# Optimization experiments

Measured on AMD Instinct MI355X. Metric: run time of the kernel, lower is better.

The kernel has to match this reference:

```python
import jax, jax.numpy as jnp
import numpy as np

WINDOW_SIZE = 11
SIGMA = 1.5
WEIGHTS = np.array([0.0448, 0.2856, 0.3001, 0.2363, 0.1333], dtype=np.float32)
LEVELS = 5


def _gaussian(ws, sigma):
    x = np.arange(ws, dtype=np.float32)
    g = np.exp(-((x - ws // 2) ** 2) / (2.0 * sigma ** 2))
    return g / g.sum()


def _window3d(ws, channel):
    g = _gaussian(ws, SIGMA)
    w3 = np.einsum('i,j,k->ijk', g, g, g).astype(np.float32)  # [ws,ws,ws]
    # OIDHW, depthwise: O=channel, I=1
    return jnp.asarray(np.broadcast_to(w3[None, None], (channel, 1, ws, ws, ws)))


def _conv3d(x, w, channel):
    return jax.lax.conv_general_dilated(
        x, w, window_strides=(1, 1, 1), padding='VALID',
        dimension_numbers=('NCDHW', 'OIDHW', 'NCDHW'),
        feature_group_count=channel)


def _avg_pool3d(x):
    s = jax.lax.reduce_window(x, 0.0, jax.lax.add,
                              (1, 1, 2, 2, 2), (1, 1, 2, 2, 2), 'VALID')
    return s / 8.0


def _ssim(img1, img2, window_size):
    _, channel, d, h, w = img1.shape
    # val_range=None branch: L derived from img1 statistics
    max_val = jnp.where(jnp.max(img1) > 128, 255.0, 1.0)
    min_val = jnp.where(jnp.min(img1) < -0.5, -1.0, 0.0)
    L = max_val - min_val
    real_size = min(window_size, d, h, w)
    win = _window3d(real_size, channel)

    mu1 = _conv3d(img1, win, channel)
    mu2 = _conv3d(img2, win, channel)
    mu1_sq = mu1 * mu1
    mu2_sq = mu2 * mu2
    mu1_mu2 = mu1 * mu2
    sigma1_sq = _conv3d(img1 * img1, win, channel) - mu1_sq
    sigma2_sq = _conv3d(img2 * img2, win, channel) - mu2_sq
    sigma12 = _conv3d(img1 * img2, win, channel) - mu1_mu2

    C1 = (0.01 * L) ** 2
    C2 = (0.03 * L) ** 2
    v1 = 2.0 * sigma12 + C2
    v2 = sigma1_sq + sigma2_sq + C2
    cs = jnp.mean(v1 / v2)
    ssim_map = (2.0 * mu1_mu2 + C1) * v1 / ((mu1_sq + mu2_sq + C1) * v2)
    return jnp.mean(ssim_map), cs


def setup_inputs() -> dict:
    key = jax.random.key(0)
    k1, k2 = jax.random.split(key)
    shape = (2, 1, 192, 192, 192)
    img1 = jax.random.normal(k1, shape, dtype=jnp.float32)
    img2 = jax.random.normal(k2, shape, dtype=jnp.float32)
    return {"img1": img1, "img2": img2}


def reference(img1, img2):
    weights = jnp.asarray(WEIGHTS)
    ssims, mcs = [], []
    for _ in range(LEVELS):
        sim, cs = _ssim(img1, img2, WINDOW_SIZE)
        ssims.append(sim)
        mcs.append(cs)
        img1 = _avg_pool3d(img1)
        img2 = _avg_pool3d(img2)
    ssims = jnp.stack(ssims)
    mcs = jnp.stack(mcs)
    pow1 = mcs ** weights
    pow2 = ssims ** weights
    return jnp.prod(pow1[:-1]) * pow2[-1]
```

## Files before the change

kernel.cpp:

```cpp
#include <hip/hip_runtime.h>
#include <math.h>


typedef float f2 __attribute__((ext_vector_type(2)));
#define PKFMA(a, b, c) __builtin_elementwise_fma((a), (b), (c))

__device__ __forceinline__ f2 mkf2(float x, float y) { f2 r; r.x = x; r.y = y; return r; }

__device__ __forceinline__ unsigned enc_f(float f) {
    unsigned u = __float_as_uint(f);
    return (u & 0x80000000u) ? ~u : (u | 0x80000000u);
}
__device__ __forceinline__ float dec_f(unsigned e) {
    unsigned u = (e & 0x80000000u) ? (e ^ 0x80000000u) : ~e;
    return __uint_as_float(u);
}

__global__ void init_kernel(float* wsf) {
    unsigned* wsu = (unsigned*)wsf;
    int t = threadIdx.x;
    if (t < 10)       wsf[t] = 0.0f;
    else if (t < 15)  wsu[t] = 0xFFFFFFFFu;
    else if (t < 20)  wsu[t] = 0u;
    else if (t == 20) wsu[t] = 0u;
}

struct PyrParams {
    const float* src[2];
    float* dst[2][4];
};

__launch_bounds__(256, 4)
__global__ void pyramid_kernel(PyrParams P, float* wsf) {
    __shared__ float L1[16 * 256];
    __shared__ float L2[512];
    __shared__ float L3[64];
    __shared__ float smn[4], smx[4];
    unsigned* wsu = (unsigned*)wsf;

    const int tid = threadIdx.x;
    int blk = blockIdx.x;
    int r = blk % 216; blk /= 216;
    int batch = blk & 1;
    int im = blk >> 1;
    const int rx = r % 6, ry = (r / 6) % 6, rz = r / 36;

    const long N0 = 192L * 192 * 192;
    const float* src = P.src[im] + (long)batch * N0;
    float* d1 = P.dst[im][0] + (long)batch * 96 * 96 * 96;
    float* d2 = P.dst[im][1] + (long)batch * 48 * 48 * 48;
    float* d3 = P.dst[im][2] + (long)batch * 24 * 24 * 24;
    float* d4 = P.dst[im][3] + (long)batch * 12 * 12 * 12;

    float mnv[5], mxv[5];
#pragma unroll
    for (int l = 0; l < 5; l++) { mnv[l] = INFINITY; mxv[l] = -INFINITY; }

    {
        const int tx2 = tid & 7;
        const int ty  = (tid >> 3) & 15;
        const int zh  = tid >> 7;
        const long D = 192, D2 = 192L * 192;
        const int gx = 2 * (rx * 16) + 4 * tx2;
        const int gy = 2 * (ry * 16 + ty);
#pragma unroll 2
        for (int it = 0; it < 8; it++) {
            const int zo = 2 * it + zh;
            const int gz = 2 * (rz * 16 + zo);
            long base = (long)gz * D2 + (long)gy * D + gx;
            float4 a00 = *(const float4*)(src + base);
            float4 a01 = *(const float4*)(src + base + D);
            float4 a10 = *(const float4*)(src + base + D2);
            float4 a11 = *(const float4*)(src + base + D2 + D);
            float lo = fminf(fminf(fminf(fminf(a00.x, a00.y), fminf(a00.z, a00.w)),
                                   fminf(fminf(a01.x, a01.y), fminf(a01.z, a01.w))),
                             fminf(fminf(fminf(a10.x, a10.y), fminf(a10.z, a10.w)),
                                   fminf(fminf(a11.x, a11.y), fminf(a11.z, a11.w))));
            float hi = fmaxf(fmaxf(fmaxf(fmaxf(a00.x, a00.y), fmaxf(a00.z, a00.w)),
                                   fmaxf(fmaxf(a01.x, a01.y), fmaxf(a01.z, a01.w))),
                             fmaxf(fmaxf(fmaxf(a10.x, a10.y), fmaxf(a10.z, a10.w)),
                                   fmaxf(fmaxf(a11.x, a11.y), fmaxf(a11.z, a11.w))));
            mnv[0] = fminf(mnv[0], lo); mxv[0] = fmaxf(mxv[0], hi);
            float s0 = (a00.x + a00.y + a01.x + a01.y +
                        a10.x + a10.y + a11.x + a11.y) * 0.125f;
            float s1 = (a00.z + a00.w + a01.z + a01.w +
                        a10.z + a10.w + a11.z + a11.w) * 0.125f;
            mnv[1] = fminf(mnv[1], fminf(s0, s1));
            mxv[1] = fmaxf(mxv[1], fmaxf(s0, s1));
            *(float2*)&d1[(long)(rz * 16 + zo) * 96 * 96 +
                          (ry * 16 + ty) * 96 + (rx * 16 + 2 * tx2)] =
                make_float2(s0, s1);
            *(float2*)&L1[zo * 256 + ty * 16 + 2 * tx2] = make_float2(s0, s1);
        }
    }
    __syncthreads();

#pragma unroll
    for (int k = 0; k < 2; k++) {
        int o = tid + (k << 8);
        int x = o & 7, y = (o >> 3) & 7, z = o >> 6;
        float s = (L1[(2 * z) * 256 + (2 * y) * 16 + 2 * x] +
                   L1[(2 * z) * 256 + (2 * y) * 16 + 2 * x + 1] +
                   L1[(2 * z) * 256 + (2 * y + 1) * 16 + 2 * x] +
                   L1[(2 * z) * 256 + (2 * y + 1) * 16 + 2 * x + 1] +
                   L1[(2 * z + 1) * 256 + (2 * y) * 16 + 2 * x] +
                   L1[(2 * z + 1) * 256 + (2 * y) * 16 + 2 * x + 1] +
                   L1[(2 * z + 1) * 256 + (2 * y + 1) * 16 + 2 * x] +
                   L1[(2 * z + 1) * 256 + (2 * y + 1) * 16 + 2 * x + 1]) * 0.125f;
        mnv[2] = fminf(mnv[2], s); mxv[2] = fmaxf(mxv[2], s);
        d2[(long)(rz * 8 + z) * 48 * 48 + (ry * 8 + y) * 48 + (rx * 8 + x)] = s;
        L2[o] = s;
    }
    __syncthreads();

    if (tid < 64) {
        int x = tid & 3, y = (tid >> 2) & 3, z = tid >> 4;
        float s = (L2[(2 * z) * 64 + (2 * y) * 8 + 2 * x] +
                   L2[(2 * z) * 64 + (2 * y) * 8 + 2 * x + 1] +
                   L2[(2 * z) * 64 + (2 * y + 1) * 8 + 2 * x] +
                   L2[(2 * z) * 64 + (2 * y + 1) * 8 + 2 * x + 1] +
                   L2[(2 * z + 1) * 64 + (2 * y) * 8 + 2 * x] +
                   L2[(2 * z + 1) * 64 + (2 * y) * 8 + 2 * x + 1] +
                   L2[(2 * z + 1) * 64 + (2 * y + 1) * 8 + 2 * x] +
                   L2[(2 * z + 1) * 64 + (2 * y + 1) * 8 + 2 * x + 1]) * 0.125f;
        mnv[3] = fminf(mnv[3], s); mxv[3] = fmaxf(mxv[3], s);
        d3[(long)(rz * 4 + z) * 24 * 24 + (ry * 4 + y) * 24 + (rx * 4 + x)] = s;
        L3[tid] = s;
    }
    __syncthreads();

    if (tid < 8) {
        int x = tid & 1, y = (tid >> 1) & 1, z = tid >> 2;
        float s = (L3[(2 * z) * 16 + (2 * y) * 4 + 2 * x] +
                   L3[(2 * z) * 16 + (2 * y) * 4 + 2 * x + 1] +
                   L3[(2 * z) * 16 + (2 * y + 1) * 4 + 2 * x] +
                   L3[(2 * z) * 16 + (2 * y + 1) * 4 + 2 * x + 1] +
                   L3[(2 * z + 1) * 16 + (2 * y) * 4 + 2 * x] +
                   L3[(2 * z + 1) * 16 + (2 * y) * 4 + 2 * x + 1] +
                   L3[(2 * z + 1) * 16 + (2 * y + 1) * 4 + 2 * x] +
                   L3[(2 * z + 1) * 16 + (2 * y + 1) * 4 + 2 * x + 1]) * 0.125f;
        mnv[4] = fminf(mnv[4], s); mxv[4] = fmaxf(mxv[4], s);
        d4[(long)(rz * 2 + z) * 12 * 12 + (ry * 2 + y) * 12 + (rx * 2 + x)] = s;
    }

    const int lane = tid & 63, w = tid >> 6;
#pragma unroll
    for (int l = 0; l < 5; l++) {
        float mn = mnv[l], mx = mxv[l];
        for (int o = 32; o; o >>= 1) {
            mn = fminf(mn, __shfl_down(mn, o));
            mx = fmaxf(mx, __shfl_down(mx, o));
        }
        __syncthreads();
        if (lane == 0) { smn[w] = mn; smx[w] = mx; }
        __syncthreads();
        if (tid == 0 && im == 0) {
            for (int i = 1; i < 4; i++) { mn = fminf(mn, smn[i]); mx = fmaxf(mx, smx[i]); }
            atomicMin(&wsu[10 + l], enc_f(mn));
            atomicMax(&wsu[15 + l], enc_f(mx));
        }
    }
}

#define TSX 16
#define TSY 32
#define EXR 42
#define EXC 26
#define SPS 26
#define NPIX (EXR * EXC)
#define TPS 17

struct AllParams {
    const float* A[5];
    const float* B[5];
    float* out;
    double cnt[5];
    int D[5], O[5], zc[5], nTx[5], nTy[5];
    int blk0[6];
    float g[11];
};

__launch_bounds__(256)
__global__ void ssim_all_kernel(AllParams P, float* wsf) {
    __shared__ __align__(16) float2 S[2][EXR * SPS];
    __shared__ __align__(16) float4 TX4[2][EXR * TPS];

    const int tid = threadIdx.x;
    const int col = tid & 15;
    const int yg  = tid >> 4;

    int level = 0;
    {
        int b = blockIdx.x;
#pragma unroll
        for (int l = 1; l < 5; l++)
            if (b >= P.blk0[l]) level = l;
    }
    int rel = blockIdx.x - P.blk0[level];
    const int D   = P.D[level];
    const int O   = P.O[level];
    const int ZC  = P.zc[level];
    const int nTx = P.nTx[level];
    const int nTy = P.nTy[level];

    const int tx = rel % nTx;  rel /= nTx;
    const int ty = rel % nTy;  rel /= nTy;
    const int batch = rel & 1;
    const int chunk = rel >> 1;

    const int oz0 = chunk * ZC;
    const int oz1 = min(oz0 + ZC, O);
    const int nplanes = oz1 - oz0 + 10;
    const int ox0 = tx * TSX;
    const int oy0 = ty * TSY;
    const int D2  = D * D;
    const float* A = P.A[level] + (long)batch * D * D2;
    const float* B = P.B[level] + (long)batch * D * D2;

    const unsigned* wsu = (const unsigned*)wsf;
    float mxv = dec_f(wsu[15 + level]);
    float mnv = dec_f(wsu[10 + level]);
    float maxval = (mxv > 128.f) ? 255.f : 1.f;
    float minval = (mnv < -0.5f) ? -1.f : 0.f;
    float Lr = maxval - minval;
    float C1 = 0.01f * Lr; C1 *= C1;
    float C2 = 0.03f * Lr; C2 *= C2;

    int  poff[5], sidx[5];
    bool pval[5];
#pragma unroll
    for (int k = 0; k < 5; k++) {
        int idx = tid + (k << 8);
        pval[k] = (idx < NPIX);
        int row = idx / EXC;
        int c   = idx - row * EXC;
        sidx[k] = row * SPS + c;
        int gy = min(oy0 + row, D - 1);
        int gx = min(ox0 + c,   D - 1);
        poff[k] = gy * D + gx;
    }

    f2 Acc2[4][11] = {};
    float ssim_acc = 0.f, cs_acc = 0.f;

    const bool vx  = (ox0 + col < O);
    const bool vy0 = vx && (oy0 + 2 * yg < O);
    const bool vy1 = vx && (oy0 + 2 * yg + 1 < O);

    float2 Pld[5];
    {
        long zoff = (long)oz0 * D2;
#pragma unroll
        for (int k = 0; k < 5; k++)
            if (pval[k]) Pld[k] = make_float2(A[zoff + poff[k]], B[zoff + poff[k]]);
    }

    for (int it = 0; it < nplanes + 2; ++it) {
        if (it < nplanes) {
            float2* Sc = S[it & 1];
#pragma unroll
            for (int k = 0; k < 5; k++)
                if (pval[k]) Sc[sidx[k]] = Pld[k];
            if (it + 1 < nplanes) {
                long zoff = (long)(oz0 + it + 1) * D2;
#pragma unroll
                for (int k = 0; k < 5; k++)
                    if (pval[k]) Pld[k] = make_float2(A[zoff + poff[k]], B[zoff + poff[k]]);
            }
        }

        if (it >= 1 && it <= nplanes && tid < EXR * 4) {
            const float2* Sc = S[(it - 1) & 1];
            float4* Tc = TX4[(it - 1) & 1];
            const int row = tid >> 2;
            const int cg  = tid & 3;
            const float4* srow = (const float4*)(Sc + row * SPS);
            f2 mm[4] = {}, qq[4] = {};
#pragma unroll
            for (int i = 0; i < 7; i++) {
                float4 qv = srow[2 * cg + i];
#pragma unroll
                for (int h = 0; h < 2; h++) {
                    const int jj = 2 * i + h;
                    float a = h ? qv.z : qv.x;
                    float b = h ? qv.w : qv.y;
                    f2 ab  = mkf2(a, b);
                    float e  = a * b;
                    float s2 = fmaf(a, a, b * b);
                    f2 se2 = mkf2(s2, e);
#pragma unroll
                    for (int cc = 0; cc < 4; cc++) {
                        const int j = jj - cc;
                        if (j >= 0 && j <= 10) {
                            f2 w = mkf2(P.g[j], P.g[j]);
                            mm[cc] = PKFMA(w, ab,  mm[cc]);
                            qq[cc] = PKFMA(w, se2, qq[cc]);
                        }
                    }
                }
            }
#pragma unroll
            for (int cc = 0; cc < 4; cc++)
                Tc[row * TPS + 4 * cg + cc] =
                    make_float4(mm[cc].x, mm[cc].y, qq[cc].x, qq[cc].y);
        }

        if (it >= 2) {
            const float4* Tc = TX4[it & 1];
            f2 acc[4] = {};
#pragma unroll
            for (int j = 0; j < 12; j++) {
                float4 q = Tc[(2 * yg + j) * TPS + col];
                float we = (j < 11) ? P.g[j]     : 0.f;
                float wo = (j > 0)  ? P.g[j - 1] : 0.f;
                f2 w = mkf2(we, wo);
                acc[0] = PKFMA(w, mkf2(q.x, q.x), acc[0]);
                acc[1] = PKFMA(w, mkf2(q.y, q.y), acc[1]);
                acc[2] = PKFMA(w, mkf2(q.z, q.z), acc[2]);
                acc[3] = PKFMA(w, mkf2(q.w, q.w), acc[3]);
            }

#pragma unroll
            for (int f = 0; f < 4; f++) {
                f2 s = acc[f];
#pragma unroll
                for (int k = 0; k < 10; k++) {
                    f2 w = mkf2(P.g[10 - k], P.g[10 - k]);
                    Acc2[f][k] = PKFMA(w, s, Acc2[f][k + 1]);
                }
                Acc2[f][10] = mkf2(P.g[0], P.g[0]) * s;
            }

            if (it >= 12) {
#pragma unroll
                for (int r = 0; r < 2; r++) {
                    bool valid = r ? vy1 : vy0;
                    if (!valid) continue;
                    float m1v = r ? Acc2[0][0].y : Acc2[0][0].x;
                    float m2v = r ? Acc2[1][0].y : Acc2[1][0].x;
                    float sqv = r ? Acc2[2][0].y : Acc2[2][0].x;
                    float sbv = r ? Acc2[3][0].y : Acc2[3][0].x;
                    float mu11 = m1v * m1v, mu22 = m2v * m2v, mu12 = m1v * m2v;
                    float sg12 = sbv - mu12;
                    float sgs  = sqv - mu11 - mu22;
                    float v1 = 2.f * sg12 + C2;
                    float v2 = sgs + C2;
                    cs_acc   += v1 / v2;
                    ssim_acc += ((2.f * mu12 + C1) * v1) / ((mu11 + mu22 + C1) * v2);
                }
            }
        }

        __syncthreads();
    }

    float2* RED = (float2*)&S[0][0];
    RED[tid] = make_float2(ssim_acc, cs_acc);
    __syncthreads();
    for (int s = 128; s > 0; s >>= 1) {
        if (tid < s) {
            RED[tid].x += RED[tid + s].x;
            RED[tid].y += RED[tid + s].y;
        }
        __syncthreads();
    }
    if (tid == 0) {
        atomicAdd(&wsf[level],     RED[0].x);
        atomicAdd(&wsf[5 + level], RED[0].y);
        __threadfence();
        unsigned prev = atomicAdd((unsigned*)wsf + 20, 1u);
        if (prev == (unsigned)(P.blk0[5] - 1)) {
            double w[5];
            w[0] = (double)0.0448f; w[1] = (double)0.2856f; w[2] = (double)0.3001f;
            w[3] = (double)0.2363f; w[4] = (double)0.1333f;
            double prod = 1.0;
            for (int l = 0; l < 4; l++) {
                float cs = atomicAdd(&wsf[5 + l], 0.0f);
                prod *= pow((double)cs / P.cnt[l], w[l]);
            }
            float sm = atomicAdd(&wsf[4], 0.0f);
            prod *= pow((double)sm / P.cnt[4], w[4]);
            P.out[0] = (float)prod;
        }
    }
}

extern "C" void kernel_launch(void* const* d_in, const int* in_sizes, int n_in,
                              void* d_out, int out_size, void* d_ws, size_t ws_size,
                              hipStream_t stream) {
    (void)in_sizes; (void)n_in; (void)out_size; (void)ws_size;
    const float* img1 = (const float*)d_in[0];
    const float* img2 = (const float*)d_in[1];
    float* wsf = (float*)d_ws;
    float* out = (float*)d_out;

    const int Ds[5]  = {192, 96, 48, 24, 12};
    const int ZCs[5] = {46, 26, 14, 14, 2};

    float* bufA[5] = {nullptr};
    float* bufB[5] = {nullptr};
    size_t o = 32;
    for (int l = 1; l < 5; l++) {
        long n = 2L * Ds[l] * Ds[l] * Ds[l];
        bufA[l] = wsf + o; o += (size_t)n;
        bufB[l] = wsf + o; o += (size_t)n;
    }

    init_kernel<<<1, 64, 0, stream>>>(wsf);

    PyrParams PP;
    PP.src[0] = img1; PP.src[1] = img2;
    for (int l = 1; l < 5; l++) { PP.dst[0][l - 1] = bufA[l]; PP.dst[1][l - 1] = bufB[l]; }
    pyramid_kernel<<<216 * 2 * 2, 256, 0, stream>>>(PP, wsf);

    AllParams P;
    P.A[0] = img1; P.B[0] = img2;
    for (int l = 1; l < 5; l++) { P.A[l] = bufA[l]; P.B[l] = bufB[l]; }
    P.out = out;
    int acc = 0;
    for (int l = 0; l < 5; l++) {
        int D = Ds[l], O = D - 10, ZC = ZCs[l];
        int nTx = (O + TSX - 1) / TSX;
        int nTy = (O + TSY - 1) / TSY;
        int ZCn = (O + ZC - 1) / ZC;
        P.D[l] = D; P.O[l] = O; P.zc[l] = ZC; P.nTx[l] = nTx; P.nTy[l] = nTy;
        P.blk0[l] = acc;
        acc += nTx * nTy * 2 * ZCn;
        double Od = (double)O;
        P.cnt[l] = 2.0 * Od * Od * Od;
    }
    P.blk0[5] = acc;

    {
        float s = 0.f;
        for (int i = 0; i < 11; i++) {
            float d = (float)(i - 5);
            P.g[i] = expf(-d * d / 4.5f);
            s += P.g[i];
        }
        for (int i = 0; i < 11; i++) P.g[i] /= s;
    }

    ssim_all_kernel<<<acc, 256, 0, stream>>>(P, wsf);
}
```

Measured before the change: 303.4 us.

## Fuse pyramid into SSIM kernel with counter-based dependency and separate minmax pass

The pyramid downsampling is merged into the SSIM kernel as its first block range. Level-0 SSIM blocks can then run while pyramid blocks are still working, and level>0 blocks spin on a global completion counter. The level-0 min/max is moved into a separate grid-stride minmax kernel so level-0 SSIM no longer waits for the pyramid. This removes a kernel boundary and overlaps pyramid work with the level-0 convolution. The cost is an extra full read of img1, shared-memory union sizing, and a spin-wait that relies on pyramid blocks being scheduled before the waiting blocks.

```diff
diff --git a/kernel.cpp b/kernel.cpp
--- a/kernel.cpp
+++ b/kernel.cpp
@@ -21,144 +21,32 @@
     int t = threadIdx.x;
     if (t < 10)       wsf[t] = 0.0f;
     else if (t < 15)  wsu[t] = 0xFFFFFFFFu;
-    else if (t < 20)  wsu[t] = 0u;
-    else if (t == 20) wsu[t] = 0u;
-}
-
-struct PyrParams {
-    const float* src[2];
-    float* dst[2][4];
-};
-
-__launch_bounds__(256, 4)
-__global__ void pyramid_kernel(PyrParams P, float* wsf) {
-    __shared__ float L1[16 * 256];
-    __shared__ float L2[512];
-    __shared__ float L3[64];
+    else if (t < 22)  wsu[t] = 0u;
+}
+
+__global__ void minmax_kernel(const float* img1, float* wsf) {
+    unsigned* wsu = (unsigned*)wsf;
     __shared__ float smn[4], smx[4];
-    unsigned* wsu = (unsigned*)wsf;
-
-    const int tid = threadIdx.x;
-    int blk = blockIdx.x;
-    int r = blk % 216; blk /= 216;
-    int batch = blk & 1;
-    int im = blk >> 1;
-    const int rx = r % 6, ry = (r / 6) % 6, rz = r / 36;
-
-    const long N0 = 192L * 192 * 192;
-    const float* src = P.src[im] + (long)batch * N0;
-    float* d1 = P.dst[im][0] + (long)batch * 96 * 96 * 96;
-    float* d2 = P.dst[im][1] + (long)batch * 48 * 48 * 48;
-    float* d3 = P.dst[im][2] + (long)batch * 24 * 24 * 24;
-    float* d4 = P.dst[im][3] + (long)batch * 12 * 12 * 12;
-
-    float mnv[5], mxv[5];
-#pragma unroll
-    for (int l = 0; l < 5; l++) { mnv[l] = INFINITY; mxv[l] = -INFINITY; }
-
-    {
-        const int tx2 = tid & 7;
-        const int ty  = (tid >> 3) & 15;
-        const int zh  = tid >> 7;
-        const long D = 192, D2 = 192L * 192;
-        const int gx = 2 * (rx * 16) + 4 * tx2;
-        const int gy = 2 * (ry * 16 + ty);
-#pragma unroll 2
-        for (int it = 0; it < 8; it++) {
-            const int zo = 2 * it + zh;
-            const int gz = 2 * (rz * 16 + zo);
-            long base = (long)gz * D2 + (long)gy * D + gx;
-            float4 a00 = *(const float4*)(src + base);
-            float4 a01 = *(const float4*)(src + base + D);
-            float4 a10 = *(const float4*)(src + base + D2);
-            float4 a11 = *(const float4*)(src + base + D2 + D);
-            float lo = fminf(fminf(fminf(fminf(a00.x, a00.y), fminf(a00.z, a00.w)),
-                                   fminf(fminf(a01.x, a01.y), fminf(a01.z, a01.w))),
-                             fminf(fminf(fminf(a10.x, a10.y), fminf(a10.z, a10.w)),
-                                   fminf(fminf(a11.x, a11.y), fminf(a11.z, a11.w))));
-            float hi = fmaxf(fmaxf(fmaxf(fmaxf(a00.x, a00.y), fmaxf(a00.z, a00.w)),
-                                   fmaxf(fmaxf(a01.x, a01.y), fmaxf(a01.z, a01.w))),
-                             fmaxf(fmaxf(fmaxf(a10.x, a10.y), fmaxf(a10.z, a10.w)),
-                                   fmaxf(fmaxf(a11.x, a11.y), fmaxf(a11.z, a11.w))));
-            mnv[0] = fminf(mnv[0], lo); mxv[0] = fmaxf(mxv[0], hi);
-            float s0 = (a00.x + a00.y + a01.x + a01.y +
-                        a10.x + a10.y + a11.x + a11.y) * 0.125f;
-            float s1 = (a00.z + a00.w + a01.z + a01.w +
-                        a10.z + a10.w + a11.z + a11.w) * 0.125f;
-            mnv[1] = fminf(mnv[1], fminf(s0, s1));
-            mxv[1] = fmaxf(mxv[1], fmaxf(s0, s1));
-            *(float2*)&d1[(long)(rz * 16 + zo) * 96 * 96 +
-                          (ry * 16 + ty) * 96 + (rx * 16 + 2 * tx2)] =
-                make_float2(s0, s1);
-            *(float2*)&L1[zo * 256 + ty * 16 + 2 * tx2] = make_float2(s0, s1);
-        }
-    }
+    const long N4 = 2L * 192 * 192 * 192 / 4;
+    const float4* p = (const float4*)img1;
+    float mn = INFINITY, mx = -INFINITY;
+    for (long i = (long)blockIdx.x * 256 + threadIdx.x; i < N4;
+         i += (long)gridDim.x * 256) {
+        float4 v = p[i];
+        mn = fminf(mn, fminf(fminf(v.x, v.y), fminf(v.z, v.w)));
+        mx = fmaxf(mx, fmaxf(fmaxf(v.x, v.y), fmaxf(v.z, v.w)));
+    }
+    for (int o = 32; o; o >>= 1) {
+        mn = fminf(mn, __shfl_down(mn, o));
+        mx = fmaxf(mx, __shfl_down(mx, o));
+    }
+    const int lane = threadIdx.x & 63, w = threadIdx.x >> 6;
+    if (lane == 0) { smn[w] = mn; smx[w] = mx; }
     __syncthreads();
-
-#pragma unroll
-    for (int k = 0; k < 2; k++) {
-        int o = tid + (k << 8);
-        int x = o & 7, y = (o >> 3) & 7, z = o >> 6;
-        float s = (L1[(2 * z) * 256 + (2 * y) * 16 + 2 * x] +
-                   L1[(2 * z) * 256 + (2 * y) * 16 + 2 * x + 1] +
-                   L1[(2 * z) * 256 + (2 * y + 1) * 16 + 2 * x] +
-                   L1[(2 * z) * 256 + (2 * y + 1) * 16 + 2 * x + 1] +
-                   L1[(2 * z + 1) * 256 + (2 * y) * 16 + 2 * x] +
-                   L1[(2 * z + 1) * 256 + (2 * y) * 16 + 2 * x + 1] +
-                   L1[(2 * z + 1) * 256 + (2 * y + 1) * 16 + 2 * x] +
-                   L1[(2 * z + 1) * 256 + (2 * y + 1) * 16 + 2 * x + 1]) * 0.125f;
-        mnv[2] = fminf(mnv[2], s); mxv[2] = fmaxf(mxv[2], s);
-        d2[(long)(rz * 8 + z) * 48 * 48 + (ry * 8 + y) * 48 + (rx * 8 + x)] = s;
-        L2[o] = s;
-    }
-    __syncthreads();
-
-    if (tid < 64) {
-        int x = tid & 3, y = (tid >> 2) & 3, z = tid >> 4;
-        float s = (L2[(2 * z) * 64 + (2 * y) * 8 + 2 * x] +
-                   L2[(2 * z) * 64 + (2 * y) * 8 + 2 * x + 1] +
-                   L2[(2 * z) * 64 + (2 * y + 1) * 8 + 2 * x] +
-                   L2[(2 * z) * 64 + (2 * y + 1) * 8 + 2 * x + 1] +
-                   L2[(2 * z + 1) * 64 + (2 * y) * 8 + 2 * x] +
-                   L2[(2 * z + 1) * 64 + (2 * y) * 8 + 2 * x + 1] +
-                   L2[(2 * z + 1) * 64 + (2 * y + 1) * 8 + 2 * x] +
-                   L2[(2 * z + 1) * 64 + (2 * y + 1) * 8 + 2 * x + 1]) * 0.125f;
-        mnv[3] = fminf(mnv[3], s); mxv[3] = fmaxf(mxv[3], s);
-        d3[(long)(rz * 4 + z) * 24 * 24 + (ry * 4 + y) * 24 + (rx * 4 + x)] = s;
-        L3[tid] = s;
-    }
-    __syncthreads();
-
-    if (tid < 8) {
-        int x = tid & 1, y = (tid >> 1) & 1, z = tid >> 2;
-        float s = (L3[(2 * z) * 16 + (2 * y) * 4 + 2 * x] +
-                   L3[(2 * z) * 16 + (2 * y) * 4 + 2 * x + 1] +
-                   L3[(2 * z) * 16 + (2 * y + 1) * 4 + 2 * x] +
-                   L3[(2 * z) * 16 + (2 * y + 1) * 4 + 2 * x + 1] +
-                   L3[(2 * z + 1) * 16 + (2 * y) * 4 + 2 * x] +
-                   L3[(2 * z + 1) * 16 + (2 * y) * 4 + 2 * x + 1] +
-                   L3[(2 * z + 1) * 16 + (2 * y + 1) * 4 + 2 * x] +
-                   L3[(2 * z + 1) * 16 + (2 * y + 1) * 4 + 2 * x + 1]) * 0.125f;
-        mnv[4] = fminf(mnv[4], s); mxv[4] = fmaxf(mxv[4], s);
-        d4[(long)(rz * 2 + z) * 12 * 12 + (ry * 2 + y) * 12 + (rx * 2 + x)] = s;
-    }
-
-    const int lane = tid & 63, w = tid >> 6;
-#pragma unroll
-    for (int l = 0; l < 5; l++) {
-        float mn = mnv[l], mx = mxv[l];
-        for (int o = 32; o; o >>= 1) {
-            mn = fminf(mn, __shfl_down(mn, o));
-            mx = fmaxf(mx, __shfl_down(mx, o));
-        }
-        __syncthreads();
-        if (lane == 0) { smn[w] = mn; smx[w] = mx; }
-        __syncthreads();
-        if (tid == 0 && im == 0) {
-            for (int i = 1; i < 4; i++) { mn = fminf(mn, smn[i]); mx = fmaxf(mx, smx[i]); }
-            atomicMin(&wsu[10 + l], enc_f(mn));
-            atomicMax(&wsu[15 + l], enc_f(mx));
-        }
+    if (threadIdx.x == 0) {
+        for (int i = 1; i < 4; i++) { mn = fminf(mn, smn[i]); mx = fmaxf(mx, smx[i]); }
+        atomicMin(&wsu[10], enc_f(mn));
+        atomicMax(&wsu[15], enc_f(mx));
     }
 }
 
@@ -169,8 +57,9 @@
 #define SPS 26
 #define NPIX (EXR * EXC)
 #define TPS 17
-
-struct AllParams {
+#define NPYR (216 * 2 * 2)
+
+struct FusedParams {
     const float* A[5];
     const float* B[5];
     float* out;
@@ -178,25 +67,166 @@
     int D[5], O[5], zc[5], nTx[5], nTy[5];
     int blk0[6];
     float g[11];
+    const float* psrc[2];
+    float* pdst[2][4];
 };
 
 __launch_bounds__(256)
-__global__ void ssim_all_kernel(AllParams P, float* wsf) {
-    __shared__ __align__(16) float2 S[2][EXR * SPS];
-    __shared__ __align__(16) float4 TX4[2][EXR * TPS];
-
+__global__ void fused_kernel(FusedParams P, float* wsf) {
+    __shared__ __align__(16) char Ubuf[40320];
+    unsigned* wsu = (unsigned*)wsf;
     const int tid = threadIdx.x;
+
+    if (blockIdx.x < NPYR) {
+        float* L1  = (float*)Ubuf;
+        float* L2  = L1 + 4096;
+        float* L3  = L2 + 512;
+        float* smn = L3 + 64;
+        float* smx = smn + 4;
+
+        int blk = blockIdx.x;
+        int r = blk % 216; blk /= 216;
+        int batch = blk & 1;
+        int im = blk >> 1;
+        const int rx = r % 6, ry = (r / 6) % 6, rz = r / 36;
+
+        const long N0 = 192L * 192 * 192;
+        const float* src = P.psrc[im] + (long)batch * N0;
+        float* d1 = P.pdst[im][0] + (long)batch * 96 * 96 * 96;
+        float* d2 = P.pdst[im][1] + (long)batch * 48 * 48 * 48;
+        float* d3 = P.pdst[im][2] + (long)batch * 24 * 24 * 24;
+        float* d4 = P.pdst[im][3] + (long)batch * 12 * 12 * 12;
+
+        float mnv[5], mxv[5];
+#pragma unroll
+        for (int l = 1; l < 5; l++) { mnv[l] = INFINITY; mxv[l] = -INFINITY; }
+
+        {
+            const int tx2 = tid & 7;
+            const int ty  = (tid >> 3) & 15;
+            const int zh  = tid >> 7;
+            const long D = 192, D2 = 192L * 192;
+            const int gx = 2 * (rx * 16) + 4 * tx2;
+            const int gy = 2 * (ry * 16 + ty);
+#pragma unroll 2
+            for (int it = 0; it < 8; it++) {
+                const int zo = 2 * it + zh;
+                const int gz = 2 * (rz * 16 + zo);
+                long base = (long)gz * D2 + (long)gy * D + gx;
+                float4 a00 = *(const float4*)(src + base);
+                float4 a01 = *(const float4*)(src + base + D);
+                float4 a10 = *(const float4*)(src + base + D2);
+                float4 a11 = *(const float4*)(src + base + D2 + D);
+                float s0 = (a00.x + a00.y + a01.x + a01.y +
+                            a10.x + a10.y + a11.x + a11.y) * 0.125f;
+                float s1 = (a00.z + a00.w + a01.z + a01.w +
+                            a10.z + a10.w + a11.z + a11.w) * 0.125f;
+                mnv[1] = fminf(mnv[1], fminf(s0, s1));
+                mxv[1] = fmaxf(mxv[1], fmaxf(s0, s1));
+                *(float2*)&d1[(long)(rz * 16 + zo) * 96 * 96 +
+                              (ry * 16 + ty) * 96 + (rx * 16 + 2 * tx2)] =
+                    make_float2(s0, s1);
+                *(float2*)&L1[zo * 256 + ty * 16 + 2 * tx2] = make_float2(s0, s1);
+            }
+        }
+        __syncthreads();
+
+#pragma unroll
+        for (int k = 0; k < 2; k++) {
+            int o = tid + (k << 8);
+            int x = o & 7, y = (o >> 3) & 7, z = o >> 6;
+            float s = (L1[(2 * z) * 256 + (2 * y) * 16 + 2 * x] +
+                       L1[(2 * z) * 256 + (2 * y) * 16 + 2 * x + 1] +
+                       L1[(2 * z) * 256 + (2 * y + 1) * 16 + 2 * x] +
+                       L1[(2 * z) * 256 + (2 * y + 1) * 16 + 2 * x + 1] +
+                       L1[(2 * z + 1) * 256 + (2 * y) * 16 + 2 * x] +
+                       L1[(2 * z + 1) * 256 + (2 * y) * 16 + 2 * x + 1] +
+                       L1[(2 * z + 1) * 256 + (2 * y + 1) * 16 + 2 * x] +
+                       L1[(2 * z + 1) * 256 + (2 * y + 1) * 16 + 2 * x + 1]) * 0.125f;
+            mnv[2] = fminf(mnv[2], s); mxv[2] = fmaxf(mxv[2], s);
+            d2[(long)(rz * 8 + z) * 48 * 48 + (ry * 8 + y) * 48 + (rx * 8 + x)] = s;
+            L2[o] = s;
+        }
+        __syncthreads();
+
+        if (tid < 64) {
+            int x = tid & 3, y = (tid >> 2) & 3, z = tid >> 4;
+            float s = (L2[(2 * z) * 64 + (2 * y) * 8 + 2 * x] +
+                       L2[(2 * z) * 64 + (2 * y) * 8 + 2 * x + 1] +
+                       L2[(2 * z) * 64 + (2 * y + 1) * 8 + 2 * x] +
+                       L2[(2 * z) * 64 + (2 * y + 1) * 8 + 2 * x + 1] +
+                       L2[(2 * z + 1) * 64 + (2 * y) * 8 + 2 * x] +
+                       L2[(2 * z + 1) * 64 + (2 * y) * 8 + 2 * x + 1] +
+                       L2[(2 * z + 1) * 64 + (2 * y + 1) * 8 + 2 * x] +
+                       L2[(2 * z + 1) * 64 + (2 * y + 1) * 8 + 2 * x + 1]) * 0.125f;
+            mnv[3] = fminf(mnv[3], s); mxv[3] = fmaxf(mxv[3], s);
+            d3[(long)(rz * 4 + z) * 24 * 24 + (ry * 4 + y) * 24 + (rx * 4 + x)] = s;
+            L3[tid] = s;
+        }
+        __syncthreads();
+
+        if (tid < 8) {
+            int x = tid & 1, y = (tid >> 1) & 1, z = tid >> 2;
+            float s = (L3[(2 * z) * 16 + (2 * y) * 4 + 2 * x] +
+                       L3[(2 * z) * 16 + (2 * y) * 4 + 2 * x + 1] +
+                       L3[(2 * z) * 16 + (2 * y + 1) * 4 + 2 * x] +
+                       L3[(2 * z) * 16 + (2 * y + 1) * 4 + 2 * x + 1] +
+                       L3[(2 * z + 1) * 16 + (2 * y) * 4 + 2 * x] +
+                       L3[(2 * z + 1) * 16 + (2 * y) * 4 + 2 * x + 1] +
+                       L3[(2 * z + 1) * 16 + (2 * y + 1) * 4 + 2 * x] +
+                       L3[(2 * z + 1) * 16 + (2 * y + 1) * 4 + 2 * x + 1]) * 0.125f;
+            mnv[4] = fminf(mnv[4], s); mxv[4] = fmaxf(mxv[4], s);
+            d4[(long)(rz * 2 + z) * 12 * 12 + (ry * 2 + y) * 12 + (rx * 2 + x)] = s;
+        }
+
+        const int lane = tid & 63, w = tid >> 6;
+#pragma unroll
+        for (int l = 1; l < 5; l++) {
+            float mn = mnv[l], mx = mxv[l];
+            for (int o = 32; o; o >>= 1) {
+                mn = fminf(mn, __shfl_down(mn, o));
+                mx = fmaxf(mx, __shfl_down(mx, o));
+            }
+            __syncthreads();
+            if (lane == 0) { smn[w] = mn; smx[w] = mx; }
+            __syncthreads();
+            if (tid == 0 && im == 0) {
+                for (int i = 1; i < 4; i++) { mn = fminf(mn, smn[i]); mx = fmaxf(mx, smx[i]); }
+                atomicMin(&wsu[10 + l], enc_f(mn));
+                atomicMax(&wsu[15 + l], enc_f(mx));
+            }
+        }
+
+        __syncthreads();
+        if (tid == 0) { __threadfence(); atomicAdd(&wsu[21], 1u); }
+        return;
+    }
+
+    float2* S0 = (float2*)Ubuf;
+    float2* S1 = S0 + EXR * SPS;
+    float4* T0 = (float4*)(S1 + EXR * SPS);
+    float4* T1 = T0 + EXR * TPS;
+
     const int col = tid & 15;
     const int yg  = tid >> 4;
 
     int level = 0;
     {
-        int b = blockIdx.x;
+        int b = blockIdx.x - NPYR;
 #pragma unroll
         for (int l = 1; l < 5; l++)
             if (b >= P.blk0[l]) level = l;
     }
-    int rel = blockIdx.x - P.blk0[level];
+    int rel = (blockIdx.x - NPYR) - P.blk0[level];
+
+    if (level > 0) {
+        if (tid == 0) {
+            while (atomicAdd(&wsu[21], 0u) < NPYR) __builtin_amdgcn_s_sleep(8);
+            __threadfence();
+        }
+        __syncthreads();
+    }
+
     const int D   = P.D[level];
     const int O   = P.O[level];
     const int ZC  = P.zc[level];
@@ -217,7 +247,6 @@
     const float* A = P.A[level] + (long)batch * D * D2;
     const float* B = P.B[level] + (long)batch * D * D2;
 
-    const unsigned* wsu = (const unsigned*)wsf;
     float mxv = dec_f(wsu[15 + level]);
     float mnv = dec_f(wsu[10 + level]);
     float maxval = (mxv > 128.f) ? 255.f : 1.f;
@@ -257,7 +286,7 @@
 
     for (int it = 0; it < nplanes + 2; ++it) {
         if (it < nplanes) {
-            float2* Sc = S[it & 1];
+            float2* Sc = (it & 1) ? S1 : S0;
 #pragma unroll
             for (int k = 0; k < 5; k++)
                 if (pval[k]) Sc[sidx[k]] = Pld[k];
@@ -270,8 +299,8 @@
         }
 
         if (it >= 1 && it <= nplanes && tid < EXR * 4) {
-            const float2* Sc = S[(it - 1) & 1];
-            float4* Tc = TX4[(it - 1) & 1];
+            const float2* Sc = ((it - 1) & 1) ? S1 : S0;
+            float4* Tc = ((it - 1) & 1) ? T1 : T0;
             const int row = tid >> 2;
             const int cg  = tid & 3;
             const float4* srow = (const float4*)(Sc + row * SPS);
@@ -306,7 +335,7 @@
         }
 
         if (it >= 2) {
-            const float4* Tc = TX4[it & 1];
+            const float4* Tc = (it & 1) ? T1 : T0;
             f2 acc[4] = {};
 #pragma unroll
             for (int j = 0; j < 12; j++) {
@@ -354,7 +383,7 @@
         __syncthreads();
     }
 
-    float2* RED = (float2*)&S[0][0];
+    float2* RED = (float2*)S0;
     RED[tid] = make_float2(ssim_acc, cs_acc);
     __syncthreads();
     for (int s = 128; s > 0; s >>= 1) {
@@ -368,7 +397,7 @@
         atomicAdd(&wsf[level],     RED[0].x);
         atomicAdd(&wsf[5 + level], RED[0].y);
         __threadfence();
-        unsigned prev = atomicAdd((unsigned*)wsf + 20, 1u);
+        unsigned prev = atomicAdd(&wsu[20], 1u);
         if (prev == (unsigned)(P.blk0[5] - 1)) {
             double w[5];
             w[0] = (double)0.0448f; w[1] = (double)0.2856f; w[2] = (double)0.3001f;
@@ -407,16 +436,14 @@
     }
 
     init_kernel<<<1, 64, 0, stream>>>(wsf);
-
-    PyrParams PP;
-    PP.src[0] = img1; PP.src[1] = img2;
-    for (int l = 1; l < 5; l++) { PP.dst[0][l - 1] = bufA[l]; PP.dst[1][l - 1] = bufB[l]; }
-    pyramid_kernel<<<216 * 2 * 2, 256, 0, stream>>>(PP, wsf);
-
-    AllParams P;
+    minmax_kernel<<<1024, 256, 0, stream>>>(img1, wsf);
+
+    FusedParams P;
     P.A[0] = img1; P.B[0] = img2;
     for (int l = 1; l < 5; l++) { P.A[l] = bufA[l]; P.B[l] = bufB[l]; }
     P.out = out;
+    P.psrc[0] = img1; P.psrc[1] = img2;
+    for (int l = 1; l < 5; l++) { P.pdst[0][l - 1] = bufA[l]; P.pdst[1][l - 1] = bufB[l]; }
     int acc = 0;
     for (int l = 0; l < 5; l++) {
         int D = Ds[l], O = D - 10, ZC = ZCs[l];
@@ -441,5 +468,5 @@
         for (int i = 0; i < 11; i++) P.g[i] /= s;
     }
 
-    ssim_all_kernel<<<acc, 256, 0, stream>>>(P, wsf);
-}
+    fused_kernel<<<NPYR + acc, 256, 0, stream>>>(P, wsf);
+}
```

Result: slower. 369.1 us (+21.6%).
